# Performance work log

Measured on AMD Instinct MI355X. Metric: run time of the kernel, lower is better.

Reference implementation:

```python
import jax, jax.numpy as jnp
import numpy as np

N_NODES = 50000
N_EDGES = 600000
EMB_DIM = 128
HIDDEN = 128
BN_EPS = 1e-5


def setup_inputs() -> dict:
    key = jax.random.key(0)
    ks = jax.random.split(key, 8)
    s_in = 1.0 / np.sqrt(EMB_DIM)
    s_h = 1.0 / np.sqrt(HIDDEN)
    return {
        "x_idx": jnp.arange(N_NODES, dtype=jnp.int32),
        "edge_index": jax.random.randint(ks[0], (2, N_EDGES), 0, N_NODES, dtype=jnp.int32),
        "emb_table": jax.random.normal(ks[1], (N_NODES, EMB_DIM), jnp.float32),
        # ClusterGCNConv: lin_out (bias=False) and lin_root (bias=False)
        "W_out": jax.random.uniform(ks[2], (HIDDEN, EMB_DIM), jnp.float32, -s_in, s_in),
        "W_root": jax.random.uniform(ks[3], (HIDDEN, EMB_DIM), jnp.float32, -s_in, s_in),
        "bn0_gamma": jnp.ones((HIDDEN,), jnp.float32),
        "bn0_beta": jnp.zeros((HIDDEN,), jnp.float32),
        # SGConv 1 (K=1, add_self_loops=True, Linear with bias)
        "W_sg1": jax.random.uniform(ks[4], (HIDDEN, HIDDEN), jnp.float32, -s_h, s_h),
        "b_sg1": jnp.zeros((HIDDEN,), jnp.float32),
        "bn1_gamma": jnp.ones((HIDDEN,), jnp.float32),
        "bn1_beta": jnp.zeros((HIDDEN,), jnp.float32),
        # SGConv 2 (final layer)
        "W_sg2": jax.random.uniform(ks[5], (HIDDEN, HIDDEN), jnp.float32, -s_h, s_h),
        "b_sg2": jnp.zeros((HIDDEN,), jnp.float32),
    }


def _cluster_gcn(x, row, col, W_out, W_root, n):
    # PyG ClusterGCNConv (add_self_loops=False, diag_lambda=0, bias=False):
    # out[c] = sum_{(r->c)} (1/deg(c)) * x[r];  return out @ W_out^T + x @ W_root^T
    deg = jax.ops.segment_sum(jnp.ones_like(col, dtype=x.dtype), col, num_segments=n)
    deg_inv = 1.0 / jnp.maximum(deg, 1.0)
    msg = x[row] * deg_inv[col][:, None]                  # [E, D]
    agg = jax.ops.segment_sum(msg, col, num_segments=n)   # [N, D]
    return agg @ W_out.T + x @ W_root.T


def _sg_conv(x, row, col, W, b, n):
    # PyG SGConv K=1 with gcn_norm: A_hat = D^{-1/2}(A+I)D^{-1/2}, then Linear.
    loop = jnp.arange(n, dtype=row.dtype)
    r = jnp.concatenate([row, loop])
    c = jnp.concatenate([col, loop])
    deg = jax.ops.segment_sum(jnp.ones_like(c, dtype=x.dtype), c, num_segments=n)
    dis = jnp.where(deg > 0, jax.lax.rsqrt(jnp.maximum(deg, 1e-12)), 0.0)
    ew = dis[r] * dis[c]                                   # [E+N]
    agg = jax.ops.segment_sum(x[r] * ew[:, None], c, num_segments=n)
    return agg @ W.T + b


def _bn(x, gamma, beta):
    # BatchNorm1d in training mode: batch statistics, biased variance.
    mu = x.mean(axis=0)
    var = ((x - mu) ** 2).mean(axis=0)
    return (x - mu) * jax.lax.rsqrt(var + BN_EPS) * gamma + beta


def reference(x_idx, edge_index, emb_table, W_out, W_root, bn0_gamma, bn0_beta,
              W_sg1, b_sg1, bn1_gamma, bn1_beta, W_sg2, b_sg2):
    n = emb_table.shape[0]
    row, col = edge_index[0], edge_index[1]
    x = emb_table[x_idx]                                   # [N, D]
    # layer 0: ClusterGCNConv -> BN -> ReLU (dropout p=0)
    x = _cluster_gcn(x, row, col, W_out, W_root, n)
    x = jax.nn.relu(_bn(x, bn0_gamma, bn0_beta))
    # layer 1: SGConv -> BN -> ReLU
    x = _sg_conv(x, row, col, W_sg1, b_sg1, n)
    x = jax.nn.relu(_bn(x, bn1_gamma, bn1_beta))
    # final SGConv
    return _sg_conv(x, row, col, W_sg2, b_sg2, n)
```

## Files before the change

kernel.cpp:

```cpp
#include <hip/hip_runtime.h>
#include <stdint.h>

#define NN 50000
#define NE 600000
#define DD 128
#define BN_EPS 1e-5f

typedef __attribute__((ext_vector_type(8))) short short8;
typedef __attribute__((ext_vector_type(4))) float f32x4;

__device__ __forceinline__ float bf2f(uint16_t u) {
    union { uint32_t u; float f; } v; v.u = ((uint32_t)u) << 16; return v.f;
}
__device__ __forceinline__ uint16_t f2bf(float f) {
    union { float f; uint32_t u; } v; v.f = f;
    return (uint16_t)((v.u + 0x7FFFu + ((v.u >> 16) & 1u)) >> 16);
}
__device__ __forceinline__ float lo16(uint32_t v) { return bf2f((uint16_t)(v & 0xFFFFu)); }
__device__ __forceinline__ float hi16(uint32_t v) { return bf2f((uint16_t)(v >> 16)); }

__global__ void k_zero(uint4* __restrict__ p, int n16) {
    int i = blockIdx.x * 256 + threadIdx.x;
    if (i < n16) p[i] = make_uint4(0u, 0u, 0u, 0u);
}

__global__ void k_count(const int* __restrict__ col, int* __restrict__ cnt) {
    int e = blockIdx.x * 256 + threadIdx.x;
    if (e < NE) atomicAdd(&cnt[col[e]], 1);
}

__global__ void k_alloc(const int* __restrict__ cnt, int* __restrict__ cursor,
                        int* __restrict__ off, int* __restrict__ fillp,
                        float* __restrict__ deginv, float* __restrict__ dis) {
    int i = blockIdx.x * 256 + threadIdx.x;
    int lane = threadIdx.x & 63;
    int deg = (i < NN) ? cnt[i] : 0;
    int v = deg;
    #pragma unroll
    for (int d = 1; d < 64; d <<= 1) {
        int t = __shfl_up(v, d, 64);
        if (lane >= d) v += t;
    }
    int total = __shfl(v, 63, 64);
    int wbase = 0;
    if (lane == 63) wbase = atomicAdd(cursor, total);
    wbase = __shfl(wbase, 63, 64);
    int base = wbase + v - deg;
    if (i < NN) {
        off[i] = base;
        fillp[i] = base;
        deginv[i] = 1.0f / fmaxf((float)deg, 1.0f);
        dis[i] = rsqrtf((float)deg + 1.0f);
    }
}

__global__ void k_fill(const int* __restrict__ ei, int* __restrict__ fillp,
                       int* __restrict__ csr_row) {
    int e = blockIdx.x * 256 + threadIdx.x;
    if (e < NE) {
        int c = ei[NE + e];
        int p = atomicAdd(&fillp[c], 1);
        csr_row[p] = ei[e];
    }
}

__global__ void k_gather(const int* __restrict__ x_idx, const float* __restrict__ emb,
                         uint16_t* __restrict__ xb) {
    int idx = blockIdx.x * 256 + threadIdx.x;
    if (idx >= NN * 32) return;
    int node = idx >> 5, c4 = (idx & 31) << 2;
    int src = x_idx[node];
    float4 v = *(const float4*)(emb + (size_t)src * DD + c4);
    ushort4 o;
    o.x = f2bf(v.x); o.y = f2bf(v.y); o.z = f2bf(v.z); o.w = f2bf(v.w);
    *(ushort4*)(xb + (size_t)node * DD + c4) = o;
}

template<int MODE>
__global__ __launch_bounds__(256)
void k_agg(const uint16_t* __restrict__ xb, const int* __restrict__ off,
           const int* __restrict__ cnt, const int* __restrict__ csr_row,
           const float* __restrict__ deginv, const float* __restrict__ dis,
           uint16_t* __restrict__ aggb) {
    int node = blockIdx.x * 4 + (threadIdx.x >> 6);
    if (node >= NN) return;
    int lane = threadIdx.x & 63;
    const uint32_t* __restrict__ xw = (const uint32_t*)xb;
    float a0 = 0.0f, a1 = 0.0f;
    if (MODE == 1) {
        uint32_t v = xw[(size_t)node * 64 + lane];
        a0 = lo16(v); a1 = hi16(v);
    }
    int s = off[node], e = s + cnt[node];
    for (int base = s; base < e; base += 64) {
        int c64 = min(e - base, 64);
        int idxv = (lane < c64) ? csr_row[base + lane] : 0;
        int i = 0;
        for (; i + 8 <= c64; i += 8) {
            uint32_t v[8];
            #pragma unroll
            for (int u = 0; u < 8; ++u) {
                int r = __builtin_amdgcn_readlane(idxv, i + u);
                v[u] = xw[(size_t)r * 64 + lane];
            }
            #pragma unroll
            for (int u = 0; u < 8; ++u) { a0 += lo16(v[u]); a1 += hi16(v[u]); }
        }
        if (i + 4 <= c64) {
            uint32_t v[4];
            #pragma unroll
            for (int u = 0; u < 4; ++u) {
                int r = __builtin_amdgcn_readlane(idxv, i + u);
                v[u] = xw[(size_t)r * 64 + lane];
            }
            #pragma unroll
            for (int u = 0; u < 4; ++u) { a0 += lo16(v[u]); a1 += hi16(v[u]); }
            i += 4;
        }
        for (; i < c64; ++i) {
            int r = __builtin_amdgcn_readlane(idxv, i);
            uint32_t v = xw[(size_t)r * 64 + lane];
            a0 += lo16(v); a1 += hi16(v);
        }
    }
    float sc = (MODE == 1) ? dis[node] : deginv[node];
    a0 *= sc; a1 *= sc;
    uint32_t o = (uint32_t)f2bf(a0) | ((uint32_t)f2bf(a1) << 16);
    *(uint32_t*)(aggb + (size_t)node * DD + lane * 2) = o;
}

template<bool DUAL, bool STATS, bool BIAS, bool STORE_BF16>
__global__ __launch_bounds__(256, 2)
void k_gemm(const uint16_t* __restrict__ A1, const uint16_t* __restrict__ A2,
            const float* __restrict__ W1, const float* __restrict__ W2,
            const float* __restrict__ bias, float* __restrict__ Hf,
            uint16_t* __restrict__ Hb, float* __restrict__ stats) {
    __shared__ uint16_t Alds[128 * 128];
    __shared__ uint16_t Wlds[128 * 128];
    const int t = threadIdx.x;
    const int lane = t & 63, wid = t >> 6;
    const int wm = (wid >> 1) * 64, wn = (wid & 1) * 64;
    const int m0 = blockIdx.x * 128;
    f32x4 zero = {0.0f, 0.0f, 0.0f, 0.0f};
    f32x4 acc[4][4];
    #pragma unroll
    for (int m = 0; m < 4; ++m)
        #pragma unroll
        for (int n = 0; n < 4; ++n) acc[m][n] = zero;

    const int NP = DUAL ? 2 : 1;
    for (int p = 0; p < NP; ++p) {
        const uint16_t* A = (DUAL && p) ? A2 : A1;
        const float* W = (DUAL && p) ? W2 : W1;
        if (p) __syncthreads();
        #pragma unroll
        for (int it = 0; it < 8; ++it) {
            int idx = it * 256 + t;
            int row = idx >> 4, c16 = idx & 15;
            uint32_t boff = (uint32_t)(row * 256 + ((c16 * 16) ^ ((row & 7) << 4)));
            uint4 v = make_uint4(0u, 0u, 0u, 0u);
            if (m0 + row < NN)
                v = *(const uint4*)(A + (size_t)(m0 + row) * DD + c16 * 8);
            *(uint4*)((char*)Alds + boff) = v;
        }
        #pragma unroll
        for (int it = 0; it < 8; ++it) {
            int idx = it * 256 + t;
            int row = idx >> 4, c8 = idx & 15;
            const float* wp = W + row * DD + c8 * 8;
            float4 v0 = *(const float4*)(wp);
            float4 v1 = *(const float4*)(wp + 4);
            uint4 pk;
            pk.x = (uint32_t)f2bf(v0.x) | ((uint32_t)f2bf(v0.y) << 16);
            pk.y = (uint32_t)f2bf(v0.z) | ((uint32_t)f2bf(v0.w) << 16);
            pk.z = (uint32_t)f2bf(v1.x) | ((uint32_t)f2bf(v1.y) << 16);
            pk.w = (uint32_t)f2bf(v1.z) | ((uint32_t)f2bf(v1.w) << 16);
            uint32_t boff = (uint32_t)(row * 256 + ((c8 * 16) ^ ((row & 7) << 4)));
            *(uint4*)((char*)Wlds + boff) = pk;
        }
        __syncthreads();
        #pragma unroll
        for (int ks = 0; ks < 4; ++ks) {
            short8 a[4], b[4];
            int kb = ks * 64 + ((lane >> 4) << 4);
            #pragma unroll
            for (int m = 0; m < 4; ++m) {
                int row = wm + m * 16 + (lane & 15);
                a[m] = *(const short8*)((const char*)Alds + row * 256 + (kb ^ ((row & 7) << 4)));
            }
            #pragma unroll
            for (int n = 0; n < 4; ++n) {
                int row = wn + n * 16 + (lane & 15);
                b[n] = *(const short8*)((const char*)Wlds + row * 256 + (kb ^ ((row & 7) << 4)));
            }
            #pragma unroll
            for (int m = 0; m < 4; ++m)
                #pragma unroll
                for (int n = 0; n < 4; ++n)
                    acc[m][n] = __builtin_amdgcn_mfma_f32_16x16x32_bf16(a[m], b[n], acc[m][n], 0, 0, 0);
        }
    }
    #pragma unroll
    for (int n = 0; n < 4; ++n) {
        int col = wn + n * 16 + (lane & 15);
        float bb = BIAS ? bias[col] : 0.0f;
        float ssum = 0.0f, ssq = 0.0f;
        #pragma unroll
        for (int m = 0; m < 4; ++m) {
            int rbase = m0 + wm + m * 16 + ((lane >> 4) << 2);
            #pragma unroll
            for (int i = 0; i < 4; ++i) {
                int gr = rbase + i;
                if (gr < NN) {
                    float v = acc[m][n][i] + bb;
                    if (STORE_BF16) Hb[(size_t)gr * DD + col] = f2bf(v);
                    else            Hf[(size_t)gr * DD + col] = v;
                    ssum += v; ssq += v * v;
                }
            }
        }
        if (STATS) {
            ssum += __shfl_xor(ssum, 16, 64);
            ssum += __shfl_xor(ssum, 32, 64);
            ssq  += __shfl_xor(ssq, 16, 64);
            ssq  += __shfl_xor(ssq, 32, 64);
            if (lane < 16) {
                atomicAdd(&stats[col], ssum);
                atomicAdd(&stats[DD + col], ssq);
            }
        }
    }
}

__global__ __launch_bounds__(256)
void k_bnrelu(const uint16_t* __restrict__ Hb, const float* __restrict__ st,
              const float* __restrict__ gamma, const float* __restrict__ beta,
              const float* __restrict__ dis, uint16_t* __restrict__ xb) {
    __shared__ float s_sc[128], s_of[128];
    int t = threadIdx.x;
    if (t < 128) {
        const float invn = 1.0f / (float)NN;
        float mean = st[t] * invn;
        float var = st[DD + t] * invn - mean * mean;
        float sc = gamma[t] * rsqrtf(var + BN_EPS);
        s_sc[t] = sc;
        s_of[t] = beta[t] - mean * sc;
    }
    __syncthreads();
    int idx = blockIdx.x * 256 + t;
    int node = idx >> 4, c8 = (idx & 15) << 3;
    if (node >= NN) return;
    float d = dis[node];
    uint4 h = *(const uint4*)(Hb + (size_t)node * DD + c8);
    uint32_t hw[4] = {h.x, h.y, h.z, h.w};
    uint32_t ow[4];
    #pragma unroll
    for (int j = 0; j < 4; ++j) {
        int c = c8 + j * 2;
        float v0 = fmaxf(lo16(hw[j]) * s_sc[c]     + s_of[c],     0.0f) * d;
        float v1 = fmaxf(hi16(hw[j]) * s_sc[c + 1] + s_of[c + 1], 0.0f) * d;
        ow[j] = (uint32_t)f2bf(v0) | ((uint32_t)f2bf(v1) << 16);
    }
    uint4 o = make_uint4(ow[0], ow[1], ow[2], ow[3]);
    *(uint4*)(xb + (size_t)node * DD + c8) = o;
}

extern "C" void kernel_launch(void* const* d_in, const int* in_sizes, int n_in,
                              void* d_out, int out_size, void* d_ws, size_t ws_size,
                              hipStream_t stream) {
    const int* x_idx   = (const int*)d_in[0];
    const int* ei      = (const int*)d_in[1];
    const float* emb   = (const float*)d_in[2];
    const float* W_out = (const float*)d_in[3];
    const float* W_root= (const float*)d_in[4];
    const float* g0    = (const float*)d_in[5];
    const float* be0   = (const float*)d_in[6];
    const float* W1    = (const float*)d_in[7];
    const float* b1    = (const float*)d_in[8];
    const float* g1    = (const float*)d_in[9];
    const float* be1   = (const float*)d_in[10];
    const float* W2    = (const float*)d_in[11];
    const float* b2    = (const float*)d_in[12];
    float* out = (float*)d_out;

    char* ws = (char*)d_ws;
    size_t o = 0;
    auto carve = [&](size_t bytes) -> void* {
        void* p = ws + o;
        o = (o + bytes + 255) & ~(size_t)255;
        return p;
    };
    int* cnt      = (int*)carve((size_t)NN * 4);
    int* cursor   = (int*)carve(4);
    float* st0    = (float*)carve(256 * 4);
    float* st1    = (float*)carve(256 * 4);
    size_t zlen = o;
    int* fillp    = (int*)carve((size_t)NN * 4);
    int* off      = (int*)carve((size_t)NN * 4);
    float* deginv = (float*)carve((size_t)NN * 4);
    float* dis    = (float*)carve((size_t)NN * 4);
    int* csr_row  = (int*)carve((size_t)NE * 4);
    uint16_t* xb  = (uint16_t*)carve((size_t)NN * DD * 2);
    uint16_t* aggb= (uint16_t*)carve((size_t)NN * DD * 2);
    uint16_t* hb  = (uint16_t*)carve((size_t)NN * DD * 2);

    const int ZB = (int)((zlen / 16 + 255) / 256);
    const int EB = (NE + 255) / 256;
    const int NB = (NN + 255) / 256;
    const int GB = (NN + 127) / 128;
    const int AB = (NN + 3) / 4;
    const int VB = (NN * 32 + 255) / 256;
    const int BB = (NN * 16 + 255) / 256;

    k_zero<<<ZB, 256, 0, stream>>>((uint4*)ws, (int)(zlen / 16));
    k_count<<<EB, 256, 0, stream>>>(ei + NE, cnt);
    k_alloc<<<NB, 256, 0, stream>>>(cnt, cursor, off, fillp, deginv, dis);
    k_fill<<<EB, 256, 0, stream>>>(ei, fillp, csr_row);
    k_gather<<<VB, 256, 0, stream>>>(x_idx, emb, xb);

    k_agg<0><<<AB, 256, 0, stream>>>(xb, off, cnt, csr_row, deginv, dis, aggb);
    k_gemm<true, true, false, true><<<GB, 256, 0, stream>>>(
        aggb, xb, W_out, W_root, nullptr, nullptr, hb, st0);
    k_bnrelu<<<BB, 256, 0, stream>>>(hb, st0, g0, be0, dis, xb);

    k_agg<1><<<AB, 256, 0, stream>>>(xb, off, cnt, csr_row, deginv, dis, aggb);
    k_gemm<false, true, true, true><<<GB, 256, 0, stream>>>(
        aggb, nullptr, W1, nullptr, b1, nullptr, hb, st1);
    k_bnrelu<<<BB, 256, 0, stream>>>(hb, st1, g1, be1, dis, xb);

    k_agg<1><<<AB, 256, 0, stream>>>(xb, off, cnt, csr_row, deginv, dis, aggb);
    k_gemm<false, false, true, false><<<GB, 256, 0, stream>>>(
        aggb, nullptr, W2, nullptr, b2, out, nullptr, nullptr);
}
```

Before: 268.7 us.

## Fuse preprocessing kernels, pre-convert weights, half-wave aggregation, direct-global A loads in GEMM

```diff
diff --git a/kernel.cpp b/kernel.cpp
--- a/kernel.cpp
+++ b/kernel.cpp
@@ -24,9 +24,40 @@
     if (i < n16) p[i] = make_uint4(0u, 0u, 0u, 0u);
 }
 
-__global__ void k_count(const int* __restrict__ col, int* __restrict__ cnt) {
-    int e = blockIdx.x * 256 + threadIdx.x;
-    if (e < NE) atomicAdd(&cnt[col[e]], 1);
+#define EB ((NE + 255) / 256)
+#define VB ((NN * 32) / 256)
+#define WB 32
+__global__ void k_pre(const int* __restrict__ ei, int* __restrict__ cnt,
+                      const int* __restrict__ x_idx, const float* __restrict__ emb,
+                      uint16_t* __restrict__ xb,
+                      const float* __restrict__ Wa, const float* __restrict__ Wb_,
+                      const float* __restrict__ Wc, const float* __restrict__ Wd,
+                      uint16_t* __restrict__ wb) {
+    int b = blockIdx.x;
+    if (b < EB) {
+        int e = b * 256 + threadIdx.x;
+        if (e < NE) atomicAdd(&cnt[ei[NE + e]], 1);
+    } else if (b < EB + VB) {
+        int idx = (b - EB) * 256 + threadIdx.x;
+        int node = idx >> 5, c4 = (idx & 31) << 2;
+        int src = x_idx[node];
+        float4 v = *(const float4*)(emb + (size_t)src * DD + c4);
+        ushort4 o;
+        o.x = f2bf(v.x); o.y = f2bf(v.y); o.z = f2bf(v.z); o.w = f2bf(v.w);
+        *(ushort4*)(xb + (size_t)node * DD + c4) = o;
+    } else {
+        int idx = (b - EB - VB) * 256 + threadIdx.x;
+        int w = idx >> 11, rem = idx & 2047;
+        const float* src = (w == 0) ? Wa : (w == 1) ? Wb_ : (w == 2) ? Wc : Wd;
+        float4 v0 = *(const float4*)(src + rem * 8);
+        float4 v1 = *(const float4*)(src + rem * 8 + 4);
+        uint4 pk;
+        pk.x = (uint32_t)f2bf(v0.x) | ((uint32_t)f2bf(v0.y) << 16);
+        pk.y = (uint32_t)f2bf(v0.z) | ((uint32_t)f2bf(v0.w) << 16);
+        pk.z = (uint32_t)f2bf(v1.x) | ((uint32_t)f2bf(v1.y) << 16);
+        pk.w = (uint32_t)f2bf(v1.z) | ((uint32_t)f2bf(v1.w) << 16);
+        *(uint4*)(wb + (size_t)w * 16384 + rem * 8) = pk;
+    }
 }
 
 __global__ void k_alloc(const int* __restrict__ cnt, int* __restrict__ cursor,
@@ -64,141 +95,136 @@
     }
 }
 
-__global__ void k_gather(const int* __restrict__ x_idx, const float* __restrict__ emb,
-                         uint16_t* __restrict__ xb) {
-    int idx = blockIdx.x * 256 + threadIdx.x;
-    if (idx >= NN * 32) return;
-    int node = idx >> 5, c4 = (idx & 31) << 2;
-    int src = x_idx[node];
-    float4 v = *(const float4*)(emb + (size_t)src * DD + c4);
-    ushort4 o;
-    o.x = f2bf(v.x); o.y = f2bf(v.y); o.z = f2bf(v.z); o.w = f2bf(v.w);
-    *(ushort4*)(xb + (size_t)node * DD + c4) = o;
-}
-
 template<int MODE>
 __global__ __launch_bounds__(256)
-void k_agg(const uint16_t* __restrict__ xb, const int* __restrict__ off,
+void k_agg(const uint16_t* __restrict__ X, const int* __restrict__ off,
            const int* __restrict__ cnt, const int* __restrict__ csr_row,
            const float* __restrict__ deginv, const float* __restrict__ dis,
            uint16_t* __restrict__ aggb) {
-    int node = blockIdx.x * 4 + (threadIdx.x >> 6);
+    int gw = blockIdx.x * 4 + (threadIdx.x >> 6);
+    int lane = threadIdx.x & 63;
+    int hl = lane & 31;
+    int node = gw * 2 + (lane >> 5);
     if (node >= NN) return;
-    int lane = threadIdx.x & 63;
-    const uint32_t* __restrict__ xw = (const uint32_t*)xb;
-    float a0 = 0.0f, a1 = 0.0f;
+    float a0 = 0.0f, a1 = 0.0f, a2 = 0.0f, a3 = 0.0f;
     if (MODE == 1) {
-        uint32_t v = xw[(size_t)node * 64 + lane];
-        a0 = lo16(v); a1 = hi16(v);
-    }
-    int s = off[node], e = s + cnt[node];
-    for (int base = s; base < e; base += 64) {
-        int c64 = min(e - base, 64);
-        int idxv = (lane < c64) ? csr_row[base + lane] : 0;
+        uint2 v = ((const uint2*)(X + (size_t)node * DD))[hl];
+        a0 = lo16(v.x); a1 = hi16(v.x); a2 = lo16(v.y); a3 = hi16(v.y);
+    }
+    int s = off[node], deg = cnt[node];
+    int degO = __shfl(deg, lane ^ 32, 64);
+    int mdeg = max(deg, degO);
+    for (int b = 0; b < mdeg; b += 32) {
+        int c32 = min(deg - b, 32);
+        int idxv = (hl < c32) ? csr_row[s + b + hl] : 0;
+        int steps = min(mdeg - b, 32);
         int i = 0;
-        for (; i + 8 <= c64; i += 8) {
-            uint32_t v[8];
+        for (; i + 8 <= steps; i += 8) {
+            uint2 v[8]; float w[8];
             #pragma unroll
             for (int u = 0; u < 8; ++u) {
-                int r = __builtin_amdgcn_readlane(idxv, i + u);
-                v[u] = xw[(size_t)r * 64 + lane];
-            }
-            #pragma unroll
-            for (int u = 0; u < 8; ++u) { a0 += lo16(v[u]); a1 += hi16(v[u]); }
-        }
-        if (i + 4 <= c64) {
-            uint32_t v[4];
+                int r = __shfl(idxv, (lane & 32) + i + u, 64);
+                w[u] = (b + i + u < deg) ? 1.0f : 0.0f;
+                v[u] = ((const uint2*)(X + (size_t)r * DD))[hl];
+            }
+            #pragma unroll
+            for (int u = 0; u < 8; ++u) {
+                a0 = fmaf(w[u], lo16(v[u].x), a0);
+                a1 = fmaf(w[u], hi16(v[u].x), a1);
+                a2 = fmaf(w[u], lo16(v[u].y), a2);
+                a3 = fmaf(w[u], hi16(v[u].y), a3);
+            }
+        }
+        if (i + 4 <= steps) {
+            uint2 v[4]; float w[4];
             #pragma unroll
             for (int u = 0; u < 4; ++u) {
-                int r = __builtin_amdgcn_readlane(idxv, i + u);
-                v[u] = xw[(size_t)r * 64 + lane];
-            }
-            #pragma unroll
-            for (int u = 0; u < 4; ++u) { a0 += lo16(v[u]); a1 += hi16(v[u]); }
+                int r = __shfl(idxv, (lane & 32) + i + u, 64);
+                w[u] = (b + i + u < deg) ? 1.0f : 0.0f;
+                v[u] = ((const uint2*)(X + (size_t)r * DD))[hl];
+            }
+            #pragma unroll
+            for (int u = 0; u < 4; ++u) {
+                a0 = fmaf(w[u], lo16(v[u].x), a0);
+                a1 = fmaf(w[u], hi16(v[u].x), a1);
+                a2 = fmaf(w[u], lo16(v[u].y), a2);
+                a3 = fmaf(w[u], hi16(v[u].y), a3);
+            }
             i += 4;
         }
-        for (; i < c64; ++i) {
-            int r = __builtin_amdgcn_readlane(idxv, i);
-            uint32_t v = xw[(size_t)r * 64 + lane];
-            a0 += lo16(v); a1 += hi16(v);
+        for (; i < steps; ++i) {
+            int r = __shfl(idxv, (lane & 32) + i, 64);
+            float w = (b + i < deg) ? 1.0f : 0.0f;
+            uint2 v = ((const uint2*)(X + (size_t)r * DD))[hl];
+            a0 = fmaf(w, lo16(v.x), a0);
+            a1 = fmaf(w, hi16(v.x), a1);
+            a2 = fmaf(w, lo16(v.y), a2);
+            a3 = fmaf(w, hi16(v.y), a3);
         }
     }
     float sc = (MODE == 1) ? dis[node] : deginv[node];
-    a0 *= sc; a1 *= sc;
-    uint32_t o = (uint32_t)f2bf(a0) | ((uint32_t)f2bf(a1) << 16);
-    *(uint32_t*)(aggb + (size_t)node * DD + lane * 2) = o;
+    a0 *= sc; a1 *= sc; a2 *= sc; a3 *= sc;
+    uint2 o;
+    o.x = (uint32_t)f2bf(a0) | ((uint32_t)f2bf(a1) << 16);
+    o.y = (uint32_t)f2bf(a2) | ((uint32_t)f2bf(a3) << 16);
+    ((uint2*)(aggb + (size_t)node * DD))[hl] = o;
 }
 
 template<bool DUAL, bool STATS, bool BIAS, bool STORE_BF16>
 __global__ __launch_bounds__(256, 2)
 void k_gemm(const uint16_t* __restrict__ A1, const uint16_t* __restrict__ A2,
-            const float* __restrict__ W1, const float* __restrict__ W2,
+            const uint16_t* __restrict__ Wb1, const uint16_t* __restrict__ Wb2,
             const float* __restrict__ bias, float* __restrict__ Hf,
             uint16_t* __restrict__ Hb, float* __restrict__ stats) {
-    __shared__ uint16_t Alds[128 * 128];
-    __shared__ uint16_t Wlds[128 * 128];
+    constexpr int NW = DUAL ? 2 : 1;
+    __shared__ uint16_t Wlds[NW * 128 * 128];
     const int t = threadIdx.x;
     const int lane = t & 63, wid = t >> 6;
     const int wm = (wid >> 1) * 64, wn = (wid & 1) * 64;
     const int m0 = blockIdx.x * 128;
-    f32x4 zero = {0.0f, 0.0f, 0.0f, 0.0f};
-    f32x4 acc[4][4];
-    #pragma unroll
-    for (int m = 0; m < 4; ++m)
-        #pragma unroll
-        for (int n = 0; n < 4; ++n) acc[m][n] = zero;
-
-    const int NP = DUAL ? 2 : 1;
-    for (int p = 0; p < NP; ++p) {
-        const uint16_t* A = (DUAL && p) ? A2 : A1;
-        const float* W = (DUAL && p) ? W2 : W1;
-        if (p) __syncthreads();
+    #pragma unroll
+    for (int w = 0; w < NW; ++w) {
+        const uint16_t* Ws = w ? Wb2 : Wb1;
         #pragma unroll
         for (int it = 0; it < 8; ++it) {
             int idx = it * 256 + t;
             int row = idx >> 4, c16 = idx & 15;
-            uint32_t boff = (uint32_t)(row * 256 + ((c16 * 16) ^ ((row & 7) << 4)));
-            uint4 v = make_uint4(0u, 0u, 0u, 0u);
-            if (m0 + row < NN)
-                v = *(const uint4*)(A + (size_t)(m0 + row) * DD + c16 * 8);
-            *(uint4*)((char*)Alds + boff) = v;
-        }
-        #pragma unroll
-        for (int it = 0; it < 8; ++it) {
-            int idx = it * 256 + t;
-            int row = idx >> 4, c8 = idx & 15;
-            const float* wp = W + row * DD + c8 * 8;
-            float4 v0 = *(const float4*)(wp);
-            float4 v1 = *(const float4*)(wp + 4);
-            uint4 pk;
-            pk.x = (uint32_t)f2bf(v0.x) | ((uint32_t)f2bf(v0.y) << 16);
-            pk.y = (uint32_t)f2bf(v0.z) | ((uint32_t)f2bf(v0.w) << 16);
-            pk.z = (uint32_t)f2bf(v1.x) | ((uint32_t)f2bf(v1.y) << 16);
-            pk.w = (uint32_t)f2bf(v1.z) | ((uint32_t)f2bf(v1.w) << 16);
-            uint32_t boff = (uint32_t)(row * 256 + ((c8 * 16) ^ ((row & 7) << 4)));
-            *(uint4*)((char*)Wlds + boff) = pk;
-        }
-        __syncthreads();
-        #pragma unroll
-        for (int ks = 0; ks < 4; ++ks) {
-            short8 a[4], b[4];
-            int kb = ks * 64 + ((lane >> 4) << 4);
-            #pragma unroll
-            for (int m = 0; m < 4; ++m) {
-                int row = wm + m * 16 + (lane & 15);
-                a[m] = *(const short8*)((const char*)Alds + row * 256 + (kb ^ ((row & 7) << 4)));
-            }
-            #pragma unroll
-            for (int n = 0; n < 4; ++n) {
-                int row = wn + n * 16 + (lane & 15);
-                b[n] = *(const short8*)((const char*)Wlds + row * 256 + (kb ^ ((row & 7) << 4)));
-            }
-            #pragma unroll
-            for (int m = 0; m < 4; ++m)
-                #pragma unroll
-                for (int n = 0; n < 4; ++n)
-                    acc[m][n] = __builtin_amdgcn_mfma_f32_16x16x32_bf16(a[m], b[n], acc[m][n], 0, 0, 0);
-        }
+            uint4 v = *(const uint4*)(Ws + row * DD + c16 * 8);
+            uint32_t boff = (uint32_t)(w * 32768 + row * 256 + ((c16 * 16) ^ ((row & 7) << 4)));
+            *(uint4*)((char*)Wlds + boff) = v;
+        }
+    }
+    __syncthreads();
+    f32x4 zero = {0.0f, 0.0f, 0.0f, 0.0f};
+    f32x4 acc[4][4];
+    #pragma unroll
+    for (int m = 0; m < 4; ++m)
+        #pragma unroll
+        for (int n = 0; n < 4; ++n) acc[m][n] = zero;
+
+    #pragma unroll
+    for (int ks = 0; ks < NW * 4; ++ks) {
+        const uint16_t* A = (DUAL && ks >= 4) ? A2 : A1;
+        const int kk = ks & 3;
+        const int kb = kk * 64 + ((lane >> 4) << 4);
+        short8 a[4], b[4];
+        #pragma unroll
+        for (int m = 0; m < 4; ++m) {
+            int row = m0 + wm + m * 16 + (lane & 15);
+            row = min(row, NN - 1);
+            a[m] = *(const short8*)(A + (size_t)row * DD + kk * 32 + ((lane >> 4) << 3));
+        }
+        #pragma unroll
+        for (int n = 0; n < 4; ++n) {
+            int row = wn + n * 16 + (lane & 15);
+            b[n] = *(const short8*)((const char*)Wlds + (ks >= 4 ? 32768 : 0)
+                                    + row * 256 + (kb ^ ((row & 7) << 4)));
+        }
+        #pragma unroll
+        for (int m = 0; m < 4; ++m)
+            #pragma unroll
+            for (int n = 0; n < 4; ++n)
+                acc[m][n] = __builtin_amdgcn_mfma_f32_16x16x32_bf16(a[m], b[n], acc[m][n], 0, 0, 0);
     }
     #pragma unroll
     for (int n = 0; n < 4; ++n) {
@@ -303,32 +329,31 @@
     uint16_t* xb  = (uint16_t*)carve((size_t)NN * DD * 2);
     uint16_t* aggb= (uint16_t*)carve((size_t)NN * DD * 2);
     uint16_t* hb  = (uint16_t*)carve((size_t)NN * DD * 2);
+    uint16_t* wb  = (uint16_t*)carve((size_t)4 * 16384 * 2);
 
     const int ZB = (int)((zlen / 16 + 255) / 256);
-    const int EB = (NE + 255) / 256;
     const int NB = (NN + 255) / 256;
     const int GB = (NN + 127) / 128;
-    const int AB = (NN + 3) / 4;
-    const int VB = (NN * 32 + 255) / 256;
+    const int AB = (NN / 2 + 3) / 4;
     const int BB = (NN * 16 + 255) / 256;
 
     k_zero<<<ZB, 256, 0, stream>>>((uint4*)ws, (int)(zlen / 16));
-    k_count<<<EB, 256, 0, stream>>>(ei + NE, cnt);
+    k_pre<<<EB + VB + WB, 256, 0, stream>>>(ei, cnt, x_idx, emb, xb,
+                                            W_out, W_root, W1, W2, wb);
     k_alloc<<<NB, 256, 0, stream>>>(cnt, cursor, off, fillp, deginv, dis);
     k_fill<<<EB, 256, 0, stream>>>(ei, fillp, csr_row);
-    k_gather<<<VB, 256, 0, stream>>>(x_idx, emb, xb);
 
     k_agg<0><<<AB, 256, 0, stream>>>(xb, off, cnt, csr_row, deginv, dis, aggb);
     k_gemm<true, true, false, true><<<GB, 256, 0, stream>>>(
-        aggb, xb, W_out, W_root, nullptr, nullptr, hb, st0);
+        aggb, xb, wb, wb + 16384, nullptr, nullptr, hb, st0);
     k_bnrelu<<<BB, 256, 0, stream>>>(hb, st0, g0, be0, dis, xb);
 
     k_agg<1><<<AB, 256, 0, stream>>>(xb, off, cnt, csr_row, deginv, dis, aggb);
     k_gemm<false, true, true, true><<<GB, 256, 0, stream>>>(
-        aggb, nullptr, W1, nullptr, b1, nullptr, hb, st1);
+        aggb, nullptr, wb + 32768, nullptr, b1, nullptr, hb, st1);
     k_bnrelu<<<BB, 256, 0, stream>>>(hb, st1, g1, be1, dis, xb);
 
     k_agg<1><<<AB, 256, 0, stream>>>(xb, off, cnt, csr_row, deginv, dis, aggb);
     k_gemm<false, false, true, false><<<GB, 256, 0, stream>>>(
-        aggb, nullptr, W2, nullptr, b2, out, nullptr, nullptr);
-}
+        aggb, nullptr, wb + 49152, nullptr, b2, out, nullptr, nullptr);
+}
```

Result: faster. 249.0 us (-7.3%).
